# Optimization experiments

Measured on AMD Instinct MI355X. Metric: run time of the kernel, lower is better.

Reference implementation:

```python
import jax, jax.numpy as jnp
import numpy as np

N = 50000      # n_nodes
E = 300000     # n_edges
R = 32         # n_relations
D = 256        # embedding_dim
H = 128        # bilstm_hidden_size (2H == D so gate dims line up, as the source requires)
I = 64         # input_dim (time-series feature dim)
B = 4096       # batch
S = 50         # seq_len
HOPS = 2       # context_hops


def setup_inputs() -> dict:
    key = jax.random.key(0)
    ks = jax.random.split(key, 20)
    sc = 0.02
    inp = {
        "ts": jax.random.normal(ks[0], (B, S, I), jnp.float32),
        "node_emb": jax.random.normal(ks[1], (N, D), jnp.float32) * sc,
        "rel_w": jax.random.normal(ks[2], (R, D), jnp.float32) * sc + 1.0,
        "gate_W": jax.random.normal(ks[3], (D, 2 * D), jnp.float32) * sc,
        "gate_b": jnp.zeros((D,), jnp.float32),
        "risk_W1": jax.random.normal(ks[4], (D, D), jnp.float32) * sc,
        "risk_b1": jnp.zeros((D,), jnp.float32),
        "risk_W2": jax.random.normal(ks[5], (D, D), jnp.float32) * sc,
        "risk_b2": jnp.zeros((D,), jnp.float32),
        # BiLSTM encoder params (torch gate order i,f,g,o), fwd + bwd directions
        "Wih_f": jax.random.normal(ks[6], (4 * H, I), jnp.float32) * sc,
        "Whh_f": jax.random.normal(ks[7], (4 * H, H), jnp.float32) * sc,
        "b_f": jnp.zeros((4 * H,), jnp.float32),
        "Wih_b": jax.random.normal(ks[8], (4 * H, I), jnp.float32) * sc,
        "Whh_b": jax.random.normal(ks[9], (4 * H, H), jnp.float32) * sc,
        "b_b": jnp.zeros((4 * H,), jnp.float32),
        "edge_index": jax.random.randint(ks[10], (2, E), 0, N, jnp.int32),
        "edge_type": jax.random.randint(ks[11], (E,), 0, R, jnp.int32),
        "node_indexes": jax.random.randint(ks[12], (B,), 0, N, jnp.int32),
    }
    return inp


def _lstm_dir(x, Wih, Whh, b, reverse):
    # x: [B, S, I] -> outputs [B, S, H]
    def step(carry, xt):
        h, c = carry
        g = xt @ Wih.T + h @ Whh.T + b          # [B, 4H]
        i, f, gg, o = jnp.split(g, 4, axis=-1)
        c = jax.nn.sigmoid(f) * c + jax.nn.sigmoid(i) * jnp.tanh(gg)
        h = jax.nn.sigmoid(o) * jnp.tanh(c)
        return (h, c), h
    h0 = jnp.zeros((x.shape[0], Whh.shape[1]), x.dtype)
    xs = jnp.swapaxes(x, 0, 1)                   # [S, B, I]
    _, hs = jax.lax.scan(step, (h0, h0), xs, reverse=reverse)
    return jnp.swapaxes(hs, 0, 1)                # [B, S, H]


def _gcn(emb, head, tail, edge_type, rel_w, n_hops):
    # relation-weighted multi-hop message passing: gather -> relation scale -> scatter-mean
    deg = jax.ops.segment_sum(jnp.ones((head.shape[0],), emb.dtype), head, num_segments=N)
    deg = jnp.clip(deg, 1.0)[:, None]
    out = emb
    acc = emb
    for _ in range(n_hops):
        msg = out[tail] * rel_w[edge_type]                      # [E, D]
        out = jax.ops.segment_sum(msg, head, num_segments=N) / deg
        acc = acc + out
    return acc / (n_hops + 1.0)


def reference(ts, node_emb, rel_w, gate_W, gate_b, risk_W1, risk_b1, risk_W2,
              risk_b2, Wih_f, Whh_f, b_f, Wih_b, Whh_b, b_b,
              edge_index, edge_type, node_indexes):
    head, tail = edge_index[0], edge_index[1]
    all_emb = _gcn(node_emb, head, tail, edge_type, rel_w, HOPS)
    struct = all_emb[node_indexes]                              # [B, D]
    # BiLSTM encoder, temporal embedding = mean over time of [B,S,2H]
    hf = _lstm_dir(ts, Wih_f, Whh_f, b_f, reverse=False)
    hb = _lstm_dir(ts, Wih_b, Whh_b, b_b, reverse=True)
    temporal = jnp.concatenate([hf, hb], axis=-1).mean(axis=1)  # [B, 2H] == [B, D]
    cat = jnp.concatenate([struct, temporal], axis=-1)          # [B, 2D]
    gate = jax.nn.sigmoid(cat @ gate_W.T + gate_b)              # [B, D]
    merged = gate * struct + (1.0 - gate) * temporal
    risk = jnp.tanh(merged @ risk_W1.T + risk_b1) @ risk_W2.T + risk_b2
    return jax.nn.sigmoid(risk.sum(axis=-1))                    # [B]
```

## Files before the change

### kernel.cpp

```cpp
#include <hip/hip_runtime.h>

#define N_NODES 50000
#define N_EDGES 300000
#define DIM 256
#define HID 128
#define INP 64
#define BATCH 4096
#define SEQ 50
#define SCAN_BLOCKS 196

typedef float f32x4 __attribute__((ext_vector_type(4)));
typedef __bf16 bf16x4 __attribute__((ext_vector_type(4)));
typedef __bf16 bf16x8 __attribute__((ext_vector_type(8)));

__device__ __forceinline__ float sigmoidf_(float x) {
    return __builtin_amdgcn_rcpf(1.0f + __expf(-x));
}
__device__ __forceinline__ float tanhf_(float x) {
    return 1.0f - 2.0f * __builtin_amdgcn_rcpf(1.0f + __expf(2.0f * x));
}


__global__ void k_hist(const int* __restrict__ head, int* __restrict__ deg) {
    int e = blockIdx.x * 256 + threadIdx.x;
    if (e < N_EDGES) atomicAdd(&deg[head[e]], 1);
}

__global__ void k_bsum(const int* __restrict__ deg, int* __restrict__ bsum) {
    __shared__ int red[256];
    int n = blockIdx.x * 256 + threadIdx.x;
    red[threadIdx.x] = (n < N_NODES) ? deg[n] : 0;
    __syncthreads();
    for (int st = 128; st > 0; st >>= 1) {
        if (threadIdx.x < st) red[threadIdx.x] += red[threadIdx.x + st];
        __syncthreads();
    }
    if (threadIdx.x == 0) bsum[blockIdx.x] = red[0];
}

__global__ void k_scanb(const int* __restrict__ bsum, int* __restrict__ boff) {
    __shared__ int s[256];
    int i = threadIdx.x;
    int v = (i < SCAN_BLOCKS) ? bsum[i] : 0;
    s[i] = v;
    __syncthreads();
    for (int st = 1; st < 256; st <<= 1) {
        int add = (i >= st) ? s[i - st] : 0;
        __syncthreads();
        s[i] += add;
        __syncthreads();
    }
    boff[i] = s[i] - v;
}

__global__ void k_scan2(const int* __restrict__ deg, const int* __restrict__ boff,
                        int* __restrict__ offsets, int* __restrict__ cursor) {
    __shared__ int s[256];
    int i = threadIdx.x;
    int n = blockIdx.x * 256 + i;
    int v = (n < N_NODES) ? deg[n] : 0;
    s[i] = v;
    __syncthreads();
    for (int st = 1; st < 256; st <<= 1) {
        int add = (i >= st) ? s[i - st] : 0;
        __syncthreads();
        s[i] += add;
        __syncthreads();
    }
    if (n < N_NODES) {
        int off = boff[blockIdx.x] + s[i] - v;
        offsets[n] = off;
        cursor[n] = off;
    }
    if (n == 0) offsets[N_NODES] = N_EDGES;
}

__global__ void k_place(const int* __restrict__ head, const int* __restrict__ tail,
                        const int* __restrict__ etype, int* __restrict__ cursor,
                        int* __restrict__ sorted) {
    int e = blockIdx.x * 256 + threadIdx.x;
    if (e >= N_EDGES) return;
    int h = head[e];
    int pos = atomicAdd(&cursor[h], 1);
    sorted[pos] = tail[e] | (etype[e] << 16);
}

__global__ void k_gather(const int* __restrict__ offsets, const int* __restrict__ sorted,
                         const float* __restrict__ relw, const float* __restrict__ src,
                         float* __restrict__ dst) {
    int tid = threadIdx.x;
    int w = tid >> 6, lane = tid & 63;
    int n = blockIdx.x * 4 + w;
    if (n >= N_NODES) return;
    int s = offsets[n], e = offsets[n + 1];
    f32x4 acc0 = (f32x4){0.f, 0.f, 0.f, 0.f};
    f32x4 acc1 = (f32x4){0.f, 0.f, 0.f, 0.f};
    f32x4 acc2 = (f32x4){0.f, 0.f, 0.f, 0.f};
    f32x4 acc3 = (f32x4){0.f, 0.f, 0.f, 0.f};
    int j = s;
    for (; j + 4 <= e; j += 4) {
        int p0 = sorted[j], p1 = sorted[j + 1], p2 = sorted[j + 2], p3 = sorted[j + 3];
        f32x4 v0 = *(const f32x4*)(src + (size_t)(p0 & 0xFFFF) * DIM + lane * 4);
        f32x4 v1 = *(const f32x4*)(src + (size_t)(p1 & 0xFFFF) * DIM + lane * 4);
        f32x4 v2 = *(const f32x4*)(src + (size_t)(p2 & 0xFFFF) * DIM + lane * 4);
        f32x4 v3 = *(const f32x4*)(src + (size_t)(p3 & 0xFFFF) * DIM + lane * 4);
        acc0 += v0 * *(const f32x4*)(relw + (p0 >> 16) * DIM + lane * 4);
        acc1 += v1 * *(const f32x4*)(relw + (p1 >> 16) * DIM + lane * 4);
        acc2 += v2 * *(const f32x4*)(relw + (p2 >> 16) * DIM + lane * 4);
        acc3 += v3 * *(const f32x4*)(relw + (p3 >> 16) * DIM + lane * 4);
    }
    for (; j < e; j++) {
        int p0 = sorted[j];
        f32x4 v0 = *(const f32x4*)(src + (size_t)(p0 & 0xFFFF) * DIM + lane * 4);
        acc0 += v0 * *(const f32x4*)(relw + (p0 >> 16) * DIM + lane * 4);
    }
    acc0 = (acc0 + acc1) + (acc2 + acc3);
    float inv = 1.0f / fmaxf((float)(e - s), 1.0f);
    *(f32x4*)(dst + (size_t)n * DIM + lane * 4) = acc0 * inv;
}

__global__ void k_gather2(const int* __restrict__ nidx, const int* __restrict__ offsets,
                          const int* __restrict__ sorted, const float* __restrict__ relw,
                          const float* __restrict__ out1, const float* __restrict__ emb,
                          float* __restrict__ structb) {
    int tid = threadIdx.x;
    int w = tid >> 6, lane = tid & 63;
    int b = blockIdx.x * 4 + w;
    int n = nidx[b];
    int s = offsets[n], e = offsets[n + 1];
    f32x4 acc0 = (f32x4){0.f, 0.f, 0.f, 0.f};
    f32x4 acc1 = (f32x4){0.f, 0.f, 0.f, 0.f};
    f32x4 acc2 = (f32x4){0.f, 0.f, 0.f, 0.f};
    f32x4 acc3 = (f32x4){0.f, 0.f, 0.f, 0.f};
    int j = s;
    for (; j + 4 <= e; j += 4) {
        int p0 = sorted[j], p1 = sorted[j + 1], p2 = sorted[j + 2], p3 = sorted[j + 3];
        f32x4 v0 = *(const f32x4*)(out1 + (size_t)(p0 & 0xFFFF) * DIM + lane * 4);
        f32x4 v1 = *(const f32x4*)(out1 + (size_t)(p1 & 0xFFFF) * DIM + lane * 4);
        f32x4 v2 = *(const f32x4*)(out1 + (size_t)(p2 & 0xFFFF) * DIM + lane * 4);
        f32x4 v3 = *(const f32x4*)(out1 + (size_t)(p3 & 0xFFFF) * DIM + lane * 4);
        acc0 += v0 * *(const f32x4*)(relw + (p0 >> 16) * DIM + lane * 4);
        acc1 += v1 * *(const f32x4*)(relw + (p1 >> 16) * DIM + lane * 4);
        acc2 += v2 * *(const f32x4*)(relw + (p2 >> 16) * DIM + lane * 4);
        acc3 += v3 * *(const f32x4*)(relw + (p3 >> 16) * DIM + lane * 4);
    }
    for (; j < e; j++) {
        int p0 = sorted[j];
        f32x4 v0 = *(const f32x4*)(out1 + (size_t)(p0 & 0xFFFF) * DIM + lane * 4);
        acc0 += v0 * *(const f32x4*)(relw + (p0 >> 16) * DIM + lane * 4);
    }
    acc0 = (acc0 + acc1) + (acc2 + acc3);
    float inv = 1.0f / fmaxf((float)(e - s), 1.0f);
    f32x4 o2 = acc0 * inv;
    f32x4 e0 = *(const f32x4*)(emb + (size_t)n * DIM + lane * 4);
    f32x4 o1 = *(const f32x4*)(out1 + (size_t)n * DIM + lane * 4);
    *(f32x4*)(structb + (size_t)b * DIM + lane * 4) = (e0 + o1 + o2) * (1.0f / 3.0f);
}

__global__ void k_w2frag(const float* __restrict__ Wih_f, const float* __restrict__ Whh_f,
                         const float* __restrict__ Wih_b, const float* __restrict__ Whh_b,
                         __bf16* __restrict__ w2) {
    int idx = blockIdx.x * 256 + threadIdx.x;
    int dir = idx / 98304;
    int rem = idx % 98304;
    int frag = rem >> 9;
    int within = rem & 511;
    int lane = within >> 3, j = within & 7;
    int kc = frag % 6;
    int wg = frag / 6;
    int g = wg & 3, w = wg >> 2;
    int n = g * 128 + w * 16 + (lane & 15);
    int k = kc * 32 + (lane >> 4) * 8 + j;
    const float* Wih = dir ? Wih_b : Wih_f;
    const float* Whh = dir ? Whh_b : Whh_f;
    float v = (k < 64) ? Wih[n * 64 + k] : Whh[n * 128 + (k - 64)];
    w2[idx] = (__bf16)v;
}

__global__ void k_packw(const float* __restrict__ W, __bf16* __restrict__ dst,
                        int K, int total) {
    int idx = blockIdx.x * 256 + threadIdx.x;
    if (idx >= total) return;
    int frag = idx >> 9, within = idx & 511;
    int lane = within >> 3, j = within & 7;
    int kcN = K >> 5;
    int kc = frag % kcN, T = frag / kcN;
    int n = T * 16 + (lane & 15);
    int k = kc * 32 + (lane >> 4) * 8 + j;
    dst[idx] = (__bf16)W[(size_t)n * K + k];
}

__launch_bounds__(512)
__global__ void k_lstm(const float* __restrict__ ts, const __bf16* __restrict__ w2frag,
                       const float* __restrict__ b_f, const float* __restrict__ b_b,
                       float* __restrict__ temporal) {
    int dir = blockIdx.y;
    int btile = blockIdx.x;
    int tid = threadIdx.x;
    int w = tid >> 6;
    int lane = tid & 63;
    int col = lane & 15, quad = lane >> 4;

    __shared__ __align__(16) __bf16 A[32][200];

    for (int i = tid; i < 32 * 128; i += 512) {
        A[i >> 7][64 + (i & 127)] = (__bf16)0.0f;
    }

    const float* bias = dir ? b_b : b_f;
    float bv[4];
#pragma unroll
    for (int g = 0; g < 4; g++) {
        bv[g] = bias[g * 128 + w * 16 + col];
    }

    const __bf16* wbase = w2frag + (size_t)dir * 98304 + (size_t)w * 12288;
    bf16x8 wreg[24];
#pragma unroll
    for (int f = 0; f < 24; f++) {
        wreg[f] = *(const bf16x8*)(wbase + (f << 9) + lane * 8);
    }

    int sm = tid >> 4, sc4 = (tid & 15) * 4;
    const float* xbase = ts + ((size_t)(btile * 32 + sm) * SEQ) * INP + sc4;
    f32x4 xpre = *(const f32x4*)(xbase + (size_t)(dir ? (SEQ - 1) : 0) * INP);

    f32x4 c_reg[2], hsum[2];
#pragma unroll
    for (int s = 0; s < 2; s++) {
        c_reg[s] = (f32x4){0.f, 0.f, 0.f, 0.f};
        hsum[s]  = (f32x4){0.f, 0.f, 0.f, 0.f};
    }
    __syncthreads();

    for (int t = 0; t < SEQ; t++) {
        {
            bf16x4 xv;
            xv[0] = (__bf16)xpre.x; xv[1] = (__bf16)xpre.y;
            xv[2] = (__bf16)xpre.z; xv[3] = (__bf16)xpre.w;
            *(bf16x4*)&A[sm][sc4] = xv;
        }
        if (t + 1 < SEQ) {
            int tt = dir ? (SEQ - 2 - t) : (t + 1);
            xpre = *(const f32x4*)(xbase + (size_t)tt * INP);
        }
        __syncthreads();

        f32x4 acc[8];
#pragma unroll
        for (int g = 0; g < 4; g++) {
            f32x4 z = (f32x4){bv[g], bv[g], bv[g], bv[g]};
            acc[g * 2] = z;
            acc[g * 2 + 1] = z;
        }
#pragma unroll
        for (int kc = 0; kc < 6; kc++) {
            bf16x8 a0 = *(const bf16x8*)&A[col][kc * 32 + quad * 8];
            bf16x8 a1 = *(const bf16x8*)&A[16 + col][kc * 32 + quad * 8];
#pragma unroll
            for (int g = 0; g < 4; g++) {
                bf16x8 bfrag = wreg[g * 6 + kc];
                acc[g * 2]     = __builtin_amdgcn_mfma_f32_16x16x32_bf16(a0, bfrag, acc[g * 2], 0, 0, 0);
                acc[g * 2 + 1] = __builtin_amdgcn_mfma_f32_16x16x32_bf16(a1, bfrag, acc[g * 2 + 1], 0, 0, 0);
            }
        }
        __syncthreads();

#pragma unroll
        for (int m = 0; m < 2; m++) {
#pragma unroll
            for (int r = 0; r < 4; r++) {
                float iv = acc[0 * 2 + m][r];
                float fv = acc[1 * 2 + m][r];
                float gv = acc[2 * 2 + m][r];
                float ov = acc[3 * 2 + m][r];
                float c = sigmoidf_(fv) * c_reg[m][r] + sigmoidf_(iv) * tanhf_(gv);
                float h = sigmoidf_(ov) * tanhf_(c);
                c_reg[m][r] = c;
                hsum[m][r] += h;
                A[m * 16 + quad * 4 + r][64 + w * 16 + col] = (__bf16)h;
            }
        }
    }

#pragma unroll
    for (int m = 0; m < 2; m++) {
#pragma unroll
        for (int r = 0; r < 4; r++) {
            int b = btile * 32 + m * 16 + quad * 4 + r;
            int j = w * 16 + col;
            temporal[(size_t)b * 256 + dir * 128 + j] = hsum[m][r] * (1.0f / SEQ);
        }
    }
}


__global__ void k_w2sum(const float* __restrict__ W2, const float* __restrict__ b2,
                        float* __restrict__ w2s) {
    int k = threadIdx.x;
    int bb = blockIdx.x;
    float s = 0.0f;
#pragma unroll
    for (int n = 0; n < 32; n++) s += W2[(size_t)(bb * 32 + n) * 256 + k];
    atomicAdd(&w2s[k], s);
    if (bb == 0) {
        __shared__ float red[256];
        red[k] = b2[k];
        __syncthreads();
        for (int st = 128; st > 0; st >>= 1) {
            if (k < st) red[k] += red[k + st];
            __syncthreads();
        }
        if (k == 0) atomicAdd(&w2s[256], red[0]);
    }
}

__launch_bounds__(256)
__global__ void k_head(const float* __restrict__ structb, const float* __restrict__ temporal,
                       const __bf16* __restrict__ gwp, const __bf16* __restrict__ w1p,
                       const float* __restrict__ gate_b, const float* __restrict__ risk_b1,
                       const float* __restrict__ w2s, float* __restrict__ out) {
    int bt = blockIdx.x;
    int tid = threadIdx.x;
    int w = tid >> 6, lane = tid & 63;
    int col = lane & 15, quad = lane >> 4;

    __shared__ __align__(16) __bf16 cat[16][520];
    __shared__ __align__(16) __bf16 mbuf[16][264];
    __shared__ float sacc[16];

    for (int i = tid; i < 16 * 512; i += 256) {
        int m = i >> 9, k = i & 511;
        int b = bt * 16 + m;
        float v = (k < 256) ? structb[(size_t)b * 256 + k]
                            : temporal[(size_t)b * 256 + (k - 256)];
        cat[m][k] = (__bf16)v;
    }
    if (tid < 16) sacc[tid] = 0.0f;
    __syncthreads();

    f32x4 acc[4];
#pragma unroll
    for (int ct = 0; ct < 4; ct++) {
        float b = gate_b[w * 64 + ct * 16 + col];
        acc[ct] = (f32x4){b, b, b, b};
    }
#pragma unroll
    for (int kc = 0; kc < 16; kc++) {
        bf16x8 a = *(const bf16x8*)&cat[col][kc * 32 + quad * 8];
#pragma unroll
        for (int ct = 0; ct < 4; ct++) {
            bf16x8 bf = *(const bf16x8*)(gwp + (((w * 4 + ct) * 16 + kc) << 9) + lane * 8);
            acc[ct] = __builtin_amdgcn_mfma_f32_16x16x32_bf16(a, bf, acc[ct], 0, 0, 0);
        }
    }
#pragma unroll
    for (int ct = 0; ct < 4; ct++) {
        int n = w * 64 + ct * 16 + col;
#pragma unroll
        for (int r = 0; r < 4; r++) {
            int m = quad * 4 + r;
            int b = bt * 16 + m;
            float g = sigmoidf_(acc[ct][r]);
            float s = structb[(size_t)b * 256 + n];
            float tm = temporal[(size_t)b * 256 + n];
            mbuf[m][n] = (__bf16)(g * s + (1.0f - g) * tm);
        }
    }
    __syncthreads();

    f32x4 acc2[4];
#pragma unroll
    for (int ct = 0; ct < 4; ct++) {
        float b = risk_b1[w * 64 + ct * 16 + col];
        acc2[ct] = (f32x4){b, b, b, b};
    }
#pragma unroll
    for (int kc = 0; kc < 8; kc++) {
        bf16x8 a = *(const bf16x8*)&mbuf[col][kc * 32 + quad * 8];
#pragma unroll
        for (int ct = 0; ct < 4; ct++) {
            bf16x8 bf = *(const bf16x8*)(w1p + (((w * 4 + ct) * 8 + kc) << 9) + lane * 8);
            acc2[ct] = __builtin_amdgcn_mfma_f32_16x16x32_bf16(a, bf, acc2[ct], 0, 0, 0);
        }
    }
    float part[4] = {0.f, 0.f, 0.f, 0.f};
#pragma unroll
    for (int ct = 0; ct < 4; ct++) {
        int n = w * 64 + ct * 16 + col;
        float wv = w2s[n];
#pragma unroll
        for (int r = 0; r < 4; r++) {
            part[r] += tanhf_(acc2[ct][r]) * wv;
        }
    }
#pragma unroll
    for (int off = 1; off < 16; off <<= 1) {
#pragma unroll
        for (int r = 0; r < 4; r++) part[r] += __shfl_xor(part[r], off, 64);
    }
    if (col == 0) {
#pragma unroll
        for (int r = 0; r < 4; r++) atomicAdd(&sacc[quad * 4 + r], part[r]);
    }
    __syncthreads();
    if (tid < 16) out[bt * 16 + tid] = sigmoidf_(sacc[tid] + w2s[256]);
}


extern "C" void kernel_launch(void* const* d_in, const int* in_sizes, int n_in,
                              void* d_out, int out_size, void* d_ws, size_t ws_size,
                              hipStream_t stream) {
    const float* ts       = (const float*)d_in[0];
    const float* node_emb = (const float*)d_in[1];
    const float* rel_w    = (const float*)d_in[2];
    const float* gate_W   = (const float*)d_in[3];
    const float* gate_b   = (const float*)d_in[4];
    const float* risk_W1  = (const float*)d_in[5];
    const float* risk_b1  = (const float*)d_in[6];
    const float* risk_W2  = (const float*)d_in[7];
    const float* risk_b2  = (const float*)d_in[8];
    const float* Wih_f    = (const float*)d_in[9];
    const float* Whh_f    = (const float*)d_in[10];
    const float* b_f      = (const float*)d_in[11];
    const float* Wih_b    = (const float*)d_in[12];
    const float* Whh_b    = (const float*)d_in[13];
    const float* b_b      = (const float*)d_in[14];
    const int* edge_index = (const int*)d_in[15];
    const int* edge_type  = (const int*)d_in[16];
    const int* node_idx   = (const int*)d_in[17];
    const int* head = edge_index;
    const int* tail = edge_index + N_EDGES;
    float* out = (float*)d_out;

    char* ws = (char*)d_ws;
    const size_t o_deg      = 0;
    const size_t o_bsum     = 200704;
    const size_t o_boff     = o_bsum + 1024;
    const size_t o_offsets  = o_boff + 1024;
    const size_t o_cursor   = o_offsets + 200960;
    const size_t o_sorted   = o_cursor + 200704;
    const size_t o_out1     = o_sorted + 1200128;
    const size_t o_temporal = o_out1 + 51200000;
    const size_t o_struct   = o_temporal + 4194304;
    const size_t o_gwp      = o_struct + 4194304;
    const size_t o_w1p      = o_gwp + 262144;
    const size_t o_w2s      = o_w1p + 131072;
    const size_t o_w2frag   = o_w2s + 2048;

    int*    deg      = (int*)(ws + o_deg);
    int*    bsum     = (int*)(ws + o_bsum);
    int*    boff     = (int*)(ws + o_boff);
    int*    offsets  = (int*)(ws + o_offsets);
    int*    cursor   = (int*)(ws + o_cursor);
    int*    sorted   = (int*)(ws + o_sorted);
    float*  out1     = (float*)(ws + o_out1);
    float*  temporal = (float*)(ws + o_temporal);
    float*  structb  = (float*)(ws + o_struct);
    __bf16* gwp      = (__bf16*)(ws + o_gwp);
    __bf16* w1p      = (__bf16*)(ws + o_w1p);
    float*  w2s      = (float*)(ws + o_w2s);
    __bf16* w2frag   = (__bf16*)(ws + o_w2frag);

    hipMemsetAsync(deg, 0, N_NODES * sizeof(int), stream);
    hipMemsetAsync(w2s, 0, 2048, stream);

    k_w2frag<<<768, 256, 0, stream>>>(Wih_f, Whh_f, Wih_b, Whh_b, w2frag);
    k_packw<<<512, 256, 0, stream>>>(gate_W, gwp, 512, 256 * 512);
    k_packw<<<256, 256, 0, stream>>>(risk_W1, w1p, 256, 256 * 256);
    k_w2sum<<<8, 256, 0, stream>>>(risk_W2, risk_b2, w2s);
    k_hist<<<(N_EDGES + 255) / 256, 256, 0, stream>>>(head, deg);
    k_bsum<<<SCAN_BLOCKS, 256, 0, stream>>>(deg, bsum);
    k_scanb<<<1, 256, 0, stream>>>(bsum, boff);
    k_scan2<<<SCAN_BLOCKS, 256, 0, stream>>>(deg, boff, offsets, cursor);
    k_place<<<(N_EDGES + 255) / 256, 256, 0, stream>>>(head, tail, edge_type, cursor, sorted);
    k_gather<<<(N_NODES + 3) / 4, 256, 0, stream>>>(offsets, sorted, rel_w, node_emb, out1);
    k_lstm<<<dim3(BATCH / 32, 2), 512, 0, stream>>>(ts, w2frag, b_f, b_b, temporal);
    k_gather2<<<BATCH / 4, 256, 0, stream>>>(node_idx, offsets, sorted, rel_w, out1, node_emb, structb);
    k_head<<<BATCH / 16, 256, 0, stream>>>(structb, temporal, gwp, w1p, gate_b, risk_b1, w2s, out);
}
```

Baseline: 357.7 us.

## Skip first-hop gather for unneeded nodes and halve LSTM batch tile

A new kernel marks the queried batch nodes and their in-neighbors, and the first-hop gather then skips every node that the second hop never reads. This cuts most of the 50k-node aggregation work, since only about 4096 times the average degree nodes are needed. Separately, the LSTM kernel processes 16 sequences per block instead of 32, doubling the grid to 512 blocks for better occupancy on the many CUs. The price is twice as many weight loads into registers per sequence and an extra flag kernel plus a larger memset.

```diff
diff --git a/kernel.cpp b/kernel.cpp
--- a/kernel.cpp
+++ b/kernel.cpp
@@ -9,8 +9,9 @@
 #define SEQ 50
 #define SCAN_BLOCKS 196
 
+typedef float f32x2 __attribute__((ext_vector_type(2)));
 typedef float f32x4 __attribute__((ext_vector_type(4)));
-typedef __bf16 bf16x4 __attribute__((ext_vector_type(4)));
+typedef __bf16 bf16x2 __attribute__((ext_vector_type(2)));
 typedef __bf16 bf16x8 __attribute__((ext_vector_type(8)));
 
 __device__ __forceinline__ float sigmoidf_(float x) {
@@ -85,13 +86,24 @@
     sorted[pos] = tail[e] | (etype[e] << 16);
 }
 
+__global__ void k_flag(const int* __restrict__ nidx, const int* __restrict__ offsets,
+                       const int* __restrict__ sorted, char* __restrict__ flag) {
+    int b = blockIdx.x * 256 + threadIdx.x;
+    if (b >= BATCH) return;
+    int n = nidx[b];
+    flag[n] = 1;
+    int s = offsets[n], e = offsets[n + 1];
+    for (int j = s; j < e; j++) flag[sorted[j] & 0xFFFF] = 1;
+}
+
 __global__ void k_gather(const int* __restrict__ offsets, const int* __restrict__ sorted,
                          const float* __restrict__ relw, const float* __restrict__ src,
-                         float* __restrict__ dst) {
+                         const char* __restrict__ flag, float* __restrict__ dst) {
     int tid = threadIdx.x;
     int w = tid >> 6, lane = tid & 63;
     int n = blockIdx.x * 4 + w;
     if (n >= N_NODES) return;
+    if (!flag[n]) return;
     int s = offsets[n], e = offsets[n + 1];
     f32x4 acc0 = (f32x4){0.f, 0.f, 0.f, 0.f};
     f32x4 acc1 = (f32x4){0.f, 0.f, 0.f, 0.f};
@@ -201,9 +213,9 @@
     int lane = tid & 63;
     int col = lane & 15, quad = lane >> 4;
 
-    __shared__ __align__(16) __bf16 A[32][200];
-
-    for (int i = tid; i < 32 * 128; i += 512) {
+    __shared__ __align__(16) __bf16 A[16][200];
+
+    for (int i = tid; i < 16 * 128; i += 512) {
         A[i >> 7][64 + (i & 127)] = (__bf16)0.0f;
     }
 
@@ -221,76 +233,61 @@
         wreg[f] = *(const bf16x8*)(wbase + (f << 9) + lane * 8);
     }
 
-    int sm = tid >> 4, sc4 = (tid & 15) * 4;
-    const float* xbase = ts + ((size_t)(btile * 32 + sm) * SEQ) * INP + sc4;
-    f32x4 xpre = *(const f32x4*)(xbase + (size_t)(dir ? (SEQ - 1) : 0) * INP);
-
-    f32x4 c_reg[2], hsum[2];
-#pragma unroll
-    for (int s = 0; s < 2; s++) {
-        c_reg[s] = (f32x4){0.f, 0.f, 0.f, 0.f};
-        hsum[s]  = (f32x4){0.f, 0.f, 0.f, 0.f};
-    }
+    int sm = tid >> 5, sc = (tid & 31) * 2;
+    const float* xbase = ts + ((size_t)(btile * 16 + sm) * SEQ) * INP + sc;
+    f32x2 xpre = *(const f32x2*)(xbase + (size_t)(dir ? (SEQ - 1) : 0) * INP);
+
+    f32x4 c_reg = (f32x4){0.f, 0.f, 0.f, 0.f};
+    f32x4 hsum  = (f32x4){0.f, 0.f, 0.f, 0.f};
+    int hoff = 64 + w * 16 + col;
     __syncthreads();
 
     for (int t = 0; t < SEQ; t++) {
         {
-            bf16x4 xv;
+            bf16x2 xv;
             xv[0] = (__bf16)xpre.x; xv[1] = (__bf16)xpre.y;
-            xv[2] = (__bf16)xpre.z; xv[3] = (__bf16)xpre.w;
-            *(bf16x4*)&A[sm][sc4] = xv;
+            *(bf16x2*)&A[sm][sc] = xv;
         }
         if (t + 1 < SEQ) {
             int tt = dir ? (SEQ - 2 - t) : (t + 1);
-            xpre = *(const f32x4*)(xbase + (size_t)tt * INP);
-        }
-        __syncthreads();
-
-        f32x4 acc[8];
+            xpre = *(const f32x2*)(xbase + (size_t)tt * INP);
+        }
+        __syncthreads();
+
+        f32x4 acc[4];
 #pragma unroll
         for (int g = 0; g < 4; g++) {
-            f32x4 z = (f32x4){bv[g], bv[g], bv[g], bv[g]};
-            acc[g * 2] = z;
-            acc[g * 2 + 1] = z;
+            acc[g] = (f32x4){bv[g], bv[g], bv[g], bv[g]};
         }
 #pragma unroll
         for (int kc = 0; kc < 6; kc++) {
             bf16x8 a0 = *(const bf16x8*)&A[col][kc * 32 + quad * 8];
-            bf16x8 a1 = *(const bf16x8*)&A[16 + col][kc * 32 + quad * 8];
 #pragma unroll
             for (int g = 0; g < 4; g++) {
-                bf16x8 bfrag = wreg[g * 6 + kc];
-                acc[g * 2]     = __builtin_amdgcn_mfma_f32_16x16x32_bf16(a0, bfrag, acc[g * 2], 0, 0, 0);
-                acc[g * 2 + 1] = __builtin_amdgcn_mfma_f32_16x16x32_bf16(a1, bfrag, acc[g * 2 + 1], 0, 0, 0);
+                acc[g] = __builtin_amdgcn_mfma_f32_16x16x32_bf16(a0, wreg[g * 6 + kc], acc[g], 0, 0, 0);
             }
         }
         __syncthreads();
 
 #pragma unroll
-        for (int m = 0; m < 2; m++) {
-#pragma unroll
-            for (int r = 0; r < 4; r++) {
-                float iv = acc[0 * 2 + m][r];
-                float fv = acc[1 * 2 + m][r];
-                float gv = acc[2 * 2 + m][r];
-                float ov = acc[3 * 2 + m][r];
-                float c = sigmoidf_(fv) * c_reg[m][r] + sigmoidf_(iv) * tanhf_(gv);
-                float h = sigmoidf_(ov) * tanhf_(c);
-                c_reg[m][r] = c;
-                hsum[m][r] += h;
-                A[m * 16 + quad * 4 + r][64 + w * 16 + col] = (__bf16)h;
-            }
-        }
-    }
-
-#pragma unroll
-    for (int m = 0; m < 2; m++) {
-#pragma unroll
         for (int r = 0; r < 4; r++) {
-            int b = btile * 32 + m * 16 + quad * 4 + r;
-            int j = w * 16 + col;
-            temporal[(size_t)b * 256 + dir * 128 + j] = hsum[m][r] * (1.0f / SEQ);
-        }
+            float iv = acc[0][r];
+            float fv = acc[1][r];
+            float gv = acc[2][r];
+            float ov = acc[3][r];
+            float c = sigmoidf_(fv) * c_reg[r] + sigmoidf_(iv) * tanhf_(gv);
+            float h = sigmoidf_(ov) * tanhf_(c);
+            c_reg[r] = c;
+            hsum[r] += h;
+            A[quad * 4 + r][hoff] = (__bf16)h;
+        }
+    }
+
+#pragma unroll
+    for (int r = 0; r < 4; r++) {
+        int b = btile * 16 + quad * 4 + r;
+        int j = w * 16 + col;
+        temporal[(size_t)b * 256 + dir * 128 + j] = hsum[r] * (1.0f / SEQ);
     }
 }
 
@@ -435,7 +432,8 @@
 
     char* ws = (char*)d_ws;
     const size_t o_deg      = 0;
-    const size_t o_bsum     = 200704;
+    const size_t o_flagbuf  = 200704;
+    const size_t o_bsum     = o_flagbuf + 50176;
     const size_t o_boff     = o_bsum + 1024;
     const size_t o_offsets  = o_boff + 1024;
     const size_t o_cursor   = o_offsets + 200960;
@@ -449,6 +447,7 @@
     const size_t o_w2frag   = o_w2s + 2048;
 
     int*    deg      = (int*)(ws + o_deg);
+    char*   flag     = (char*)(ws + o_flagbuf);
     int*    bsum     = (int*)(ws + o_bsum);
     int*    boff     = (int*)(ws + o_boff);
     int*    offsets  = (int*)(ws + o_offsets);
@@ -462,7 +461,7 @@
     float*  w2s      = (float*)(ws + o_w2s);
     __bf16* w2frag   = (__bf16*)(ws + o_w2frag);
 
-    hipMemsetAsync(deg, 0, N_NODES * sizeof(int), stream);
+    hipMemsetAsync(ws, 0, o_flagbuf + 50176, stream);
     hipMemsetAsync(w2s, 0, 2048, stream);
 
     k_w2frag<<<768, 256, 0, stream>>>(Wih_f, Whh_f, Wih_b, Whh_b, w2frag);
@@ -474,8 +473,9 @@
     k_scanb<<<1, 256, 0, stream>>>(bsum, boff);
     k_scan2<<<SCAN_BLOCKS, 256, 0, stream>>>(deg, boff, offsets, cursor);
     k_place<<<(N_EDGES + 255) / 256, 256, 0, stream>>>(head, tail, edge_type, cursor, sorted);
-    k_gather<<<(N_NODES + 3) / 4, 256, 0, stream>>>(offsets, sorted, rel_w, node_emb, out1);
-    k_lstm<<<dim3(BATCH / 32, 2), 512, 0, stream>>>(ts, w2frag, b_f, b_b, temporal);
+    k_flag<<<BATCH / 256, 256, 0, stream>>>(node_idx, offsets, sorted, flag);
+    k_gather<<<(N_NODES + 3) / 4, 256, 0, stream>>>(offsets, sorted, rel_w, node_emb, flag, out1);
+    k_lstm<<<dim3(BATCH / 16, 2), 512, 0, stream>>>(ts, w2frag, b_f, b_b, temporal);
     k_gather2<<<BATCH / 4, 256, 0, stream>>>(node_idx, offsets, sorted, rel_w, out1, node_emb, structb);
     k_head<<<BATCH / 16, 256, 0, stream>>>(structb, temporal, gwp, w1p, gate_b, risk_b1, w2s, out);
 }
```

Result: no change. 353.9 us (-1.1%).
